# Kernel optimization log

Measured on AMD Instinct MI355X. Metric: run time of the kernel, lower is better.

## Reference

```python
import jax, jax.numpy as jnp
import numpy as np

B = 128          # persons in the batch
V = 300          # visits per person (< MAX_VISITS so all kept)
MAX_VISITS = 510 # 512 - 2, hard-coded in the module
D = 256          # embedding_dim * n_heads
VOCAB = 50000
MAX_DAYS = 365


def setup_inputs() -> dict:
    key = jax.random.key(0)
    k_codes, k_times, k_emb = jax.random.split(key, 3)

    total_visits = B * V  # 38400
    v = np.arange(total_visits)
    codes_per_visit = 8 + (v % 8)                      # 8..15 codes per visit
    code_to_visit = np.repeat(v, codes_per_visit).astype(np.int32)  # sorted segment ids (sum_indices)
    total_codes = code_to_visit.shape[0]               # 441600
    visit_person = (v // V).astype(np.int32)
    visit_slot = (MAX_VISITS - V + (v % V)).astype(np.int32)  # right-aligned slots

    all_codes = jax.random.randint(k_codes, (total_codes,), 0, VOCAB, dtype=jnp.int32)
    times = jax.random.uniform(k_times, (total_visits,), dtype=jnp.float32) * (MAX_DAYS - 1)
    concept_emb = jax.random.normal(k_emb, (VOCAB, D), dtype=jnp.float32)
    pad_embedding = jnp.zeros((D,), dtype=jnp.float32)  # torch.nn.Parameter(torch.zeros(D))
    # ((1/10000) ** (1/D)) ** range(D//2)
    timescales = jnp.asarray(((1.0 / 10000.0) ** (1.0 / D)) ** np.arange(D // 2), dtype=jnp.float32)

    return {
        "all_codes": all_codes,
        "code_to_visit": jnp.asarray(code_to_visit),
        "visit_person": jnp.asarray(visit_person),
        "visit_slot": jnp.asarray(visit_slot),
        "times": times,
        "concept_emb": concept_emb,
        "pad_embedding": pad_embedding,
        "timescales": timescales,
    }


def reference(all_codes, code_to_visit, visit_person, visit_slot, times,
              concept_emb, pad_embedding, timescales):
    total_visits = visit_person.shape[0]
    d = concept_emb.shape[1]

    # concept-embedding gather: [total_codes, D]
    embedded_raw = concept_emb[all_codes]

    # per-visit segment sum (index_add_): [total_visits, D]
    summed = jax.ops.segment_sum(embedded_raw, code_to_visit,
                                 num_segments=total_visits,
                                 indices_are_sorted=True)

    # padded tensor initialised with pad_embedding, then right-aligned scatter of visits
    base = jnp.zeros((B, MAX_VISITS, d), dtype=summed.dtype) + pad_embedding
    reshaped = base.at[visit_person, visit_slot].set(summed)

    # sinusoidal time embedding: cat(sin(t*ts), cos(t*ts))
    t = jnp.clip(times, 0.0, MAX_DAYS - 1)
    ang = t[:, None] * timescales[None, :]                       # [total_visits, D/2]
    temb_un = jnp.concatenate([jnp.sin(ang), jnp.cos(ang)], 1)   # [total_visits, D]
    time_embedding = jnp.zeros((B, MAX_VISITS, d), dtype=summed.dtype)
    time_embedding = time_embedding.at[visit_person, visit_slot].set(temb_un)

    return reshaped + time_embedding
```

## Files before the change

### kernel.cpp

```cpp
#include <hip/hip_runtime.h>

#define MAXV 510
#define D4 64

typedef float floatx4 __attribute__((ext_vector_type(4)));

__device__ __forceinline__ unsigned int pack2_bf16_rne(float a, float b) {
    unsigned int ua = __builtin_bit_cast(unsigned int, a);
    unsigned int ub = __builtin_bit_cast(unsigned int, b);
    ua = (ua + 0x7FFFu + ((ua >> 16) & 1u)) >> 16;
    ub = (ub + 0x7FFFu + ((ub >> 16) & 1u)) >> 16;
    return ua | (ub << 16);
}

__global__ __launch_bounds__(256) void convert_bf16(
    const float4* __restrict__ in, uint4* __restrict__ out, int npairs) {
    int i = blockIdx.x * blockDim.x + threadIdx.x;
    if (i >= npairs) return;
    const float4 a = in[2 * i];
    const float4 b = in[2 * i + 1];
    uint4 r;
    r.x = pack2_bf16_rne(a.x, a.y);
    r.y = pack2_bf16_rne(a.z, a.w);
    r.z = pack2_bf16_rne(b.x, b.y);
    r.w = pack2_bf16_rne(b.z, b.w);
    out[i] = r;
}

__global__ __launch_bounds__(256) void build_maps(
    const int* __restrict__ c2v,
    const int* __restrict__ person,
    const int* __restrict__ slot,
    int* __restrict__ inv,
    int* __restrict__ off,
    int total_codes, int total_visits)
{
    int v = blockIdx.x * blockDim.x + threadIdx.x;
    if (v >= total_visits) return;
    inv[person[v] * MAXV + slot[v]] = v;
    int lo = 0, hi = total_codes;
    while (lo < hi) {
        int m = (lo + hi) >> 1;
        if (c2v[m] < v) lo = m + 1; else hi = m;
    }
    off[v] = lo;
    if (v == 0) off[total_visits] = total_codes;
}

__device__ __forceinline__ void acc_bf16x4(floatx4& acc, uint2 u) {
    acc.x += __builtin_bit_cast(float, u.x << 16);
    acc.y += __builtin_bit_cast(float, u.x & 0xFFFF0000u);
    acc.z += __builtin_bit_cast(float, u.y << 16);
    acc.w += __builtin_bit_cast(float, u.y & 0xFFFF0000u);
}

__global__ __launch_bounds__(256) void fused_bf16(
    const int* __restrict__ all_codes,
    const float* __restrict__ times,
    const uint2* __restrict__ embh,
    const floatx4* __restrict__ pad,
    const floatx4* __restrict__ tsc,
    const int* __restrict__ inv,
    const int* __restrict__ off,
    floatx4* __restrict__ out,
    int nslots)
{
    const int tid = threadIdx.x;
    const int w = tid >> 6;
    const int lane = tid & 63;
    const int slot_id = blockIdx.x * 4 + w;
    if (slot_id >= nslots) return;

    const int v = inv[slot_id];
    if (v < 0) {
        __builtin_nontemporal_store(pad[lane], &out[slot_id * D4 + lane]);
        return;
    }

    const int lo = off[v];
    const int cnt = off[v + 1] - lo;

    float t = times[v];
    t = fminf(fmaxf(t, 0.f), 364.f);
    const floatx4 ts = tsc[lane & 31];
    floatx4 acc;
    if (lane < 32) {
        acc.x = sinf(t * ts.x); acc.y = sinf(t * ts.y);
        acc.z = sinf(t * ts.z); acc.w = sinf(t * ts.w);
    } else {
        acc.x = cosf(t * ts.x); acc.y = cosf(t * ts.y);
        acc.z = cosf(t * ts.z); acc.w = cosf(t * ts.w);
    }

    if (cnt <= 16) {
        const int mycode = all_codes[lo + min(lane, cnt - 1)];
        uint2 e[16];
#pragma unroll
        for (int j = 0; j < 16; ++j) {
            if (j < cnt) {
                const int c = __builtin_amdgcn_readlane(mycode, j);
                e[j] = embh[(size_t)c * D4 + lane];
            }
        }
#pragma unroll
        for (int j = 0; j < 16; ++j) {
            if (j < cnt) acc_bf16x4(acc, e[j]);
        }
    } else {
        for (int i = lo; i < lo + cnt; ++i) {
            const int c = all_codes[i];
            acc_bf16x4(acc, embh[(size_t)c * D4 + lane]);
        }
    }

    __builtin_nontemporal_store(acc, &out[slot_id * D4 + lane]);
}

__global__ __launch_bounds__(256) void fused_f32(
    const int* __restrict__ all_codes,
    const float* __restrict__ times,
    const floatx4* __restrict__ emb,
    const floatx4* __restrict__ pad,
    const floatx4* __restrict__ tsc,
    const int* __restrict__ inv,
    const int* __restrict__ off,
    floatx4* __restrict__ out,
    int nslots)
{
    const int tid = threadIdx.x;
    const int w = tid >> 6;
    const int lane = tid & 63;
    const int slot_id = blockIdx.x * 4 + w;
    if (slot_id >= nslots) return;

    const int v = inv[slot_id];
    if (v < 0) {
        __builtin_nontemporal_store(pad[lane], &out[slot_id * D4 + lane]);
        return;
    }
    const int lo = off[v];
    const int hi = off[v + 1];

    float t = times[v];
    t = fminf(fmaxf(t, 0.f), 364.f);
    const floatx4 ts = tsc[lane & 31];
    floatx4 acc;
    if (lane < 32) {
        acc.x = sinf(t * ts.x); acc.y = sinf(t * ts.y);
        acc.z = sinf(t * ts.z); acc.w = sinf(t * ts.w);
    } else {
        acc.x = cosf(t * ts.x); acc.y = cosf(t * ts.y);
        acc.z = cosf(t * ts.z); acc.w = cosf(t * ts.w);
    }
    for (int i = lo; i < hi; ++i)
        acc += emb[(size_t)all_codes[i] * D4 + lane];
    __builtin_nontemporal_store(acc, &out[slot_id * D4 + lane]);
}

extern "C" void kernel_launch(void* const* d_in, const int* in_sizes, int n_in,
                              void* d_out, int out_size, void* d_ws, size_t ws_size,
                              hipStream_t stream) {
    const int*   all_codes = (const int*)d_in[0];
    const int*   c2v       = (const int*)d_in[1];
    const int*   person    = (const int*)d_in[2];
    const int*   slot      = (const int*)d_in[3];
    const float* times     = (const float*)d_in[4];
    const float* emb       = (const float*)d_in[5];
    const float* pad       = (const float*)d_in[6];
    const float* tsc       = (const float*)d_in[7];

    const int total_codes  = in_sizes[0];
    const int total_visits = in_sizes[2];
    const int emb_elems    = in_sizes[5];
    const int nslots       = out_size / 256;

    char* ws = (char*)d_ws;
    int* inv = (int*)ws;
    int* off = inv + nslots;
    size_t head = ((size_t)(nslots + total_visits + 1) * sizeof(int) + 255) & ~(size_t)255;
    unsigned short* embh = (unsigned short*)(ws + head);
    const size_t needed = head + (size_t)emb_elems * sizeof(unsigned short);

    (void)hipMemsetAsync(inv, 0xFF, (size_t)nslots * sizeof(int), stream);

    build_maps<<<(total_visits + 255) / 256, 256, 0, stream>>>(
        c2v, person, slot, inv, off, total_codes, total_visits);

    if (ws_size >= needed) {
        const int npairs = emb_elems / 8;
        convert_bf16<<<(npairs + 255) / 256, 256, 0, stream>>>(
            (const float4*)emb, (uint4*)embh, npairs);
        fused_bf16<<<(nslots + 3) / 4, 256, 0, stream>>>(
            all_codes, times, (const uint2*)embh, (const floatx4*)pad,
            (const floatx4*)tsc, inv, off, (floatx4*)d_out, nslots);
    } else {
        fused_f32<<<(nslots + 3) / 4, 256, 0, stream>>>(
            all_codes, times, (const floatx4*)emb, (const floatx4*)pad,
            (const floatx4*)tsc, inv, off, (floatx4*)d_out, nslots);
    }
}
```

Before: 171.1 us.

## Gather bf16 rows as 16-byte loads across half-waves and fold memset into conversion

The bf16 gather now has each half-wave load a full 512-byte embedding row with 16-byte per-lane loads, two codes per half per iteration. The two halves are combined with a cross-half shuffle, and the output features are remapped so each lane writes one float4. The separate hipMemsetAsync that initialised the inverse map is folded into the conversion kernel, removing one launch. This trades wider loads and fewer loop iterations for extra shuffles and a strided output mapping.

Result: faster. 161.2 us (-5.8%).

```diff
diff --git a/kernel.cpp b/kernel.cpp
--- a/kernel.cpp
+++ b/kernel.cpp
@@ -13,9 +13,25 @@
     return ua | (ub << 16);
 }
 
+__device__ __forceinline__ float bf_lo(unsigned int u) {
+    return __builtin_bit_cast(float, u << 16);
+}
+__device__ __forceinline__ float bf_hi(unsigned int u) {
+    return __builtin_bit_cast(float, u & 0xFFFF0000u);
+}
+
+__device__ __forceinline__ void acc8(floatx4& a0, floatx4& a1, uint4 u) {
+    a0.x += bf_lo(u.x); a0.y += bf_hi(u.x);
+    a0.z += bf_lo(u.y); a0.w += bf_hi(u.y);
+    a1.x += bf_lo(u.z); a1.y += bf_hi(u.z);
+    a1.z += bf_lo(u.w); a1.w += bf_hi(u.w);
+}
+
 __global__ __launch_bounds__(256) void convert_bf16(
-    const float4* __restrict__ in, uint4* __restrict__ out, int npairs) {
+    const float4* __restrict__ in, uint4* __restrict__ out, int npairs,
+    int* __restrict__ inv, int nslots) {
     int i = blockIdx.x * blockDim.x + threadIdx.x;
+    if (i < nslots) inv[i] = -1;
     if (i >= npairs) return;
     const float4 a = in[2 * i];
     const float4 b = in[2 * i + 1];
@@ -47,17 +63,10 @@
     if (v == 0) off[total_visits] = total_codes;
 }
 
-__device__ __forceinline__ void acc_bf16x4(floatx4& acc, uint2 u) {
-    acc.x += __builtin_bit_cast(float, u.x << 16);
-    acc.y += __builtin_bit_cast(float, u.x & 0xFFFF0000u);
-    acc.z += __builtin_bit_cast(float, u.y << 16);
-    acc.w += __builtin_bit_cast(float, u.y & 0xFFFF0000u);
-}
-
 __global__ __launch_bounds__(256) void fused_bf16(
     const int* __restrict__ all_codes,
     const float* __restrict__ times,
-    const uint2* __restrict__ embh,
+    const uint4* __restrict__ embh,
     const floatx4* __restrict__ pad,
     const floatx4* __restrict__ tsc,
     const int* __restrict__ inv,
@@ -68,6 +77,8 @@
     const int tid = threadIdx.x;
     const int w = tid >> 6;
     const int lane = tid & 63;
+    const int half = lane >> 5;
+    const int hl = lane & 31;
     const int slot_id = blockIdx.x * 4 + w;
     if (slot_id >= nslots) return;
 
@@ -80,40 +91,50 @@
     const int lo = off[v];
     const int cnt = off[v + 1] - lo;
 
+    floatx4 acc0 = (floatx4)(0.f);
+    floatx4 acc1 = (floatx4)(0.f);
+
+    if (cnt > 0 && cnt <= 64) {
+        const int mycode = all_codes[lo + min(lane, cnt - 1)];
+        for (int j = 0; j < cnt; j += 4) {
+            const int ja = j + half;
+            const int jb = j + 2 + half;
+            const int ca = __shfl(mycode, min(ja, cnt - 1));
+            const int cb = __shfl(mycode, min(jb, cnt - 1));
+            const uint4 ea = embh[(size_t)ca * 32 + hl];
+            const uint4 eb = embh[(size_t)cb * 32 + hl];
+            if (ja < cnt) acc8(acc0, acc1, ea);
+            if (jb < cnt) acc8(acc0, acc1, eb);
+        }
+    } else {
+        for (int j = 0; j < cnt; j += 2) {
+            const int jj = min(j + half, cnt - 1);
+            const int c = all_codes[lo + jj];
+            const uint4 e = embh[(size_t)c * 32 + hl];
+            if (j + half < cnt) acc8(acc0, acc1, e);
+        }
+    }
+
+    acc0.x += __shfl_xor(acc0.x, 32); acc0.y += __shfl_xor(acc0.y, 32);
+    acc0.z += __shfl_xor(acc0.z, 32); acc0.w += __shfl_xor(acc0.w, 32);
+    acc1.x += __shfl_xor(acc1.x, 32); acc1.y += __shfl_xor(acc1.y, 32);
+    acc1.z += __shfl_xor(acc1.z, 32); acc1.w += __shfl_xor(acc1.w, 32);
+
+    const int f = 2 * hl + half;
+    floatx4 r = half ? acc1 : acc0;
+
     float t = times[v];
     t = fminf(fmaxf(t, 0.f), 364.f);
-    const floatx4 ts = tsc[lane & 31];
-    floatx4 acc;
-    if (lane < 32) {
-        acc.x = sinf(t * ts.x); acc.y = sinf(t * ts.y);
-        acc.z = sinf(t * ts.z); acc.w = sinf(t * ts.w);
-    } else {
-        acc.x = cosf(t * ts.x); acc.y = cosf(t * ts.y);
-        acc.z = cosf(t * ts.z); acc.w = cosf(t * ts.w);
-    }
-
-    if (cnt <= 16) {
-        const int mycode = all_codes[lo + min(lane, cnt - 1)];
-        uint2 e[16];
-#pragma unroll
-        for (int j = 0; j < 16; ++j) {
-            if (j < cnt) {
-                const int c = __builtin_amdgcn_readlane(mycode, j);
-                e[j] = embh[(size_t)c * D4 + lane];
-            }
-        }
-#pragma unroll
-        for (int j = 0; j < 16; ++j) {
-            if (j < cnt) acc_bf16x4(acc, e[j]);
-        }
-    } else {
-        for (int i = lo; i < lo + cnt; ++i) {
-            const int c = all_codes[i];
-            acc_bf16x4(acc, embh[(size_t)c * D4 + lane]);
-        }
-    }
-
-    __builtin_nontemporal_store(acc, &out[slot_id * D4 + lane]);
+    const floatx4 ts = tsc[f & 31];
+    if (f < 32) {
+        r.x += sinf(t * ts.x); r.y += sinf(t * ts.y);
+        r.z += sinf(t * ts.z); r.w += sinf(t * ts.w);
+    } else {
+        r.x += cosf(t * ts.x); r.y += cosf(t * ts.y);
+        r.z += cosf(t * ts.z); r.w += cosf(t * ts.w);
+    }
+
+    __builtin_nontemporal_store(r, &out[slot_id * D4 + f]);
 }
 
 __global__ __launch_bounds__(256) void fused_f32(
@@ -181,19 +202,19 @@
     unsigned short* embh = (unsigned short*)(ws + head);
     const size_t needed = head + (size_t)emb_elems * sizeof(unsigned short);
 
-    (void)hipMemsetAsync(inv, 0xFF, (size_t)nslots * sizeof(int), stream);
-
-    build_maps<<<(total_visits + 255) / 256, 256, 0, stream>>>(
-        c2v, person, slot, inv, off, total_codes, total_visits);
-
     if (ws_size >= needed) {
         const int npairs = emb_elems / 8;
         convert_bf16<<<(npairs + 255) / 256, 256, 0, stream>>>(
-            (const float4*)emb, (uint4*)embh, npairs);
+            (const float4*)emb, (uint4*)embh, npairs, inv, nslots);
+        build_maps<<<(total_visits + 255) / 256, 256, 0, stream>>>(
+            c2v, person, slot, inv, off, total_codes, total_visits);
         fused_bf16<<<(nslots + 3) / 4, 256, 0, stream>>>(
-            all_codes, times, (const uint2*)embh, (const floatx4*)pad,
+            all_codes, times, (const uint4*)embh, (const floatx4*)pad,
             (const floatx4*)tsc, inv, off, (floatx4*)d_out, nslots);
     } else {
+        (void)hipMemsetAsync(inv, 0xFF, (size_t)nslots * sizeof(int), stream);
+        build_maps<<<(total_visits + 255) / 256, 256, 0, stream>>>(
+            c2v, person, slot, inv, off, total_codes, total_visits);
         fused_f32<<<(nslots + 3) / 4, 256, 0, stream>>>(
             all_codes, times, (const floatx4*)emb, (const floatx4*)pad,
             (const floatx4*)tsc, inv, off, (floatx4*)d_out, nslots);
```
